# Optimization experiments

Hardware: AMD Instinct MI355X
Metric: run time of the kernel (lower is better)

## Reference

```python
import jax, jax.numpy as jnp
import numpy as np

N_NODES = 50000
N_EDGES = 800000
D_IN = 96
D_HID = 256
D_OUT = 2
N_GRAPHS = 64


def _gin_conv(x, src, dst, W1, b1, W2, b2):
    # GINConv with eps=0: MLP(x + sum_{j in N(i)} x_j)
    agg = jax.ops.segment_sum(x[src], dst, num_segments=x.shape[0])
    h = x + agg
    h = jax.nn.relu(h @ W1 + b1)
    return h @ W2 + b2


def setup_inputs() -> dict:
    key = jax.random.key(0)
    ks = jax.random.split(key, 12)
    x = jax.random.normal(ks[0], (N_NODES, D_IN), dtype=jnp.float32)
    edge_index = jax.random.randint(ks[1], (2, N_EDGES), 0, N_NODES, dtype=jnp.int64)
    batch = jnp.sort(jax.random.randint(ks[2], (N_NODES,), 0, N_GRAPHS, dtype=jnp.int64))

    def lin(k, fan_in, shape):
        bound = 1.0 / np.sqrt(fan_in)
        return jax.random.uniform(k, shape, jnp.float32, -bound, bound)

    W1 = lin(ks[3], D_IN, (D_IN, D_HID)); b1 = lin(ks[4], D_IN, (D_HID,))
    W2 = lin(ks[5], D_HID, (D_HID, D_HID)); b2 = lin(ks[6], D_HID, (D_HID,))
    V1 = lin(ks[7], D_HID, (D_HID, D_HID)); c1 = lin(ks[8], D_HID, (D_HID,))
    V2 = lin(ks[9], D_HID, (D_HID, D_HID)); c2 = lin(ks[10], D_HID, (D_HID,))
    Wl = lin(ks[11], D_HID, (D_HID, D_OUT)); bl = jnp.zeros((D_OUT,), jnp.float32)
    return {"x": x, "edge_index": edge_index, "batch": batch,
            "W1": W1, "b1": b1, "W2": W2, "b2": b2,
            "V1": V1, "c1": c1, "V2": V2, "c2": c2,
            "Wl": Wl, "bl": bl}


def reference(x, edge_index, batch, W1, b1, W2, b2, V1, c1, V2, c2, Wl, bl):
    src, dst = edge_index[0], edge_index[1]
    h = jax.nn.relu(_gin_conv(x, src, dst, W1, b1, W2, b2))
    h = _gin_conv(h, src, dst, V1, c1, V2, c2)
    # global_mean_pool over batch ids
    sums = jax.ops.segment_sum(h, batch, num_segments=N_GRAPHS)
    counts = jax.ops.segment_sum(jnp.ones((h.shape[0], 1), h.dtype), batch,
                                 num_segments=N_GRAPHS)
    pooled = sums / jnp.maximum(counts, 1.0)
    # dropout p=0.1 is identity in eval mode
    return pooled @ Wl + bl
```

## Files before the change

### kernel.cpp

```cpp
#include <hip/hip_runtime.h>

#define N_NODES 50000
#define N_EDGES 800000
#define D_IN 96
#define D_HID 256
#define N_GRAPHS 64

#define SCAN_NB ((N_NODES + 255) / 256)

typedef __attribute__((ext_vector_type(8))) short bf16x8;
typedef __attribute__((ext_vector_type(4))) float f32x4;

__device__ __forceinline__ unsigned short f2bf(float f) {
    union { float f; unsigned int u; } v; v.f = f;
    unsigned int r = (v.u + 0x7FFFu + ((v.u >> 16) & 1u)) >> 16;
    return (unsigned short)r;
}
__device__ __forceinline__ float bfLo(unsigned int u) {
    union { unsigned int u; float f; } v; v.u = u << 16; return v.f;
}
__device__ __forceinline__ float bfHi(unsigned int u) {
    union { unsigned int u; float f; } v; v.u = u & 0xFFFF0000u; return v.f;
}
__device__ __forceinline__ unsigned int packbf(float a, float b) {
    return (unsigned int)f2bf(a) | ((unsigned int)f2bf(b) << 16);
}

__global__ void k_count(const int* __restrict__ dst, int* __restrict__ deg, int E) {
    int e = blockIdx.x * blockDim.x + threadIdx.x;
    if (e < E) atomicAdd(&deg[dst[e]], 1);
}

__global__ __launch_bounds__(256) void k_scan1(const int* __restrict__ deg,
                                               int* __restrict__ bsum, int n) {
    __shared__ int red[256];
    int tid = threadIdx.x;
    int i = blockIdx.x * 256 + tid;
    red[tid] = (i < n) ? deg[i] : 0;
    __syncthreads();
    for (int off = 128; off > 0; off >>= 1) {
        if (tid < off) red[tid] += red[tid + off];
        __syncthreads();
    }
    if (tid == 0) bsum[blockIdx.x] = red[0];
}

__global__ __launch_bounds__(256) void k_scan2(int* __restrict__ bsum, int nb) {
    __shared__ int s[256];
    int tid = threadIdx.x;
    int v = (tid < nb) ? bsum[tid] : 0;
    s[tid] = v;
    __syncthreads();
    for (int off = 1; off < 256; off <<= 1) {
        int t = (tid >= off) ? s[tid - off] : 0;
        __syncthreads();
        s[tid] += t;
        __syncthreads();
    }
    if (tid < nb) bsum[tid] = s[tid] - v;
}

__global__ __launch_bounds__(256) void k_scan3(const int* __restrict__ deg,
                                               const int* __restrict__ bsum,
                                               int* __restrict__ rp,
                                               int* __restrict__ wp, int n) {
    __shared__ int s[256];
    int tid = threadIdx.x;
    int i = blockIdx.x * 256 + tid;
    int v = (i < n) ? deg[i] : 0;
    s[tid] = v;
    __syncthreads();
    for (int off = 1; off < 256; off <<= 1) {
        int t = (tid >= off) ? s[tid - off] : 0;
        __syncthreads();
        s[tid] += t;
        __syncthreads();
    }
    if (i < n) {
        int excl = s[tid] - v + bsum[blockIdx.x];
        rp[i] = excl;
        wp[i] = excl;
    }
    if (blockIdx.x == 0 && tid == 0) rp[n] = N_EDGES;
}

__global__ __launch_bounds__(256) void k_scatter2(const int* __restrict__ src,
                                                  const int* __restrict__ dst,
                                                  int* __restrict__ wp,
                                                  int* __restrict__ csr, int E) {
    int range = blockIdx.x & 7;
    int chunk = blockIdx.x >> 3;
    int lo = range * (N_NODES / 8);
    int hi = (range == 7) ? N_NODES : lo + (N_NODES / 8);
    int per = (E + 255) / 256;
    int s = chunk * per;
    int e = s + per;
    if (e > E) e = E;
    for (int i = s + threadIdx.x; i < e; i += 256) {
        int d = dst[i];
        if (d >= lo && d < hi) {
            int p = atomicAdd(&wp[d], 1);
            csr[p] = src[i];
        }
    }
}

__global__ __launch_bounds__(256) void k_x2bf(const float* __restrict__ x,
                                              unsigned short* __restrict__ xb, int n4) {
    int i = blockIdx.x * 256 + threadIdx.x;
    if (i >= n4) return;
    float4 v = ((const float4*)x)[i];
    ((uint2*)xb)[i] = make_uint2(packbf(v.x, v.y), packbf(v.z, v.w));
}

#define ACCUM(acc, v)                                    \
    do {                                                 \
        acc[0] += bfLo((v).x); acc[1] += bfHi((v).x);    \
        acc[2] += bfLo((v).y); acc[3] += bfHi((v).y);    \
        acc[4] += bfLo((v).z); acc[5] += bfHi((v).z);    \
        acc[6] += bfLo((v).w); acc[7] += bfHi((v).w);    \
    } while (0)

__global__ __launch_bounds__(256) void k_agg96b(const unsigned short* __restrict__ xb,
                                                const int* __restrict__ rp,
                                                const int* __restrict__ csr,
                                                unsigned short* __restrict__ h0, int n) {
    int wid = blockIdx.x * 4 + (threadIdx.x >> 6);
    if (wid >= n) return;
    int lane = threadIdx.x & 63;
    int grp = lane / 12;
    int sub = lane % 12;
    int s = rp[wid], e = rp[wid + 1];
    const uint4* xp = (const uint4*)xb;
    float a[8] = {0.f, 0.f, 0.f, 0.f, 0.f, 0.f, 0.f, 0.f};
    float b[8] = {0.f, 0.f, 0.f, 0.f, 0.f, 0.f, 0.f, 0.f};
    if (lane < 48) {
        int j = s + grp;
        for (; j + 4 < e; j += 8) {
            int sc0 = csr[j];
            int sc1 = csr[j + 4];
            uint4 v0 = xp[(size_t)sc0 * 12 + sub];
            uint4 v1 = xp[(size_t)sc1 * 12 + sub];
            ACCUM(a, v0);
            ACCUM(b, v1);
        }
        if (j < e) {
            int sc0 = csr[j];
            uint4 v0 = xp[(size_t)sc0 * 12 + sub];
            ACCUM(a, v0);
        }
    }
#pragma unroll
    for (int i = 0; i < 8; i++) a[i] += b[i];
#pragma unroll
    for (int i = 0; i < 8; i++) a[i] += __shfl(a[i], lane + 24, 64);
#pragma unroll
    for (int i = 0; i < 8; i++) a[i] += __shfl(a[i], lane + 12, 64);
    if (lane < 12) {
        uint4 v = xp[(size_t)wid * 12 + sub];
        ACCUM(a, v);
        uint4 o;
        o.x = packbf(a[0], a[1]); o.y = packbf(a[2], a[3]);
        o.z = packbf(a[4], a[5]); o.w = packbf(a[6], a[7]);
        ((uint4*)h0)[(size_t)wid * 12 + sub] = o;
    }
}

__global__ __launch_bounds__(256) void k_agg256b(const unsigned short* __restrict__ h,
                                                 const int* __restrict__ rp,
                                                 const int* __restrict__ csr,
                                                 unsigned short* __restrict__ outb, int n) {
    int wid = blockIdx.x * 4 + (threadIdx.x >> 6);
    if (wid >= n) return;
    int lane = threadIdx.x & 63;
    int half = lane >> 5;
    int sub = lane & 31;
    int s = rp[wid], e = rp[wid + 1];
    const uint4* hp = (const uint4*)h;
    float a[8] = {0.f, 0.f, 0.f, 0.f, 0.f, 0.f, 0.f, 0.f};
    float b[8] = {0.f, 0.f, 0.f, 0.f, 0.f, 0.f, 0.f, 0.f};
    int j = s + half;
    for (; j + 2 < e; j += 4) {
        int sc0 = csr[j];
        int sc1 = csr[j + 2];
        uint4 v0 = hp[(size_t)sc0 * 32 + sub];
        uint4 v1 = hp[(size_t)sc1 * 32 + sub];
        ACCUM(a, v0);
        ACCUM(b, v1);
    }
    if (j < e) {
        int sc0 = csr[j];
        uint4 v0 = hp[(size_t)sc0 * 32 + sub];
        ACCUM(a, v0);
    }
#pragma unroll
    for (int i = 0; i < 8; i++) a[i] += b[i];
#pragma unroll
    for (int i = 0; i < 8; i++) a[i] += __shfl(a[i], sub + 32, 64);
    if (half == 0) {
        uint4 v = hp[(size_t)wid * 32 + sub];
        ACCUM(a, v);
        uint4 o;
        o.x = packbf(a[0], a[1]); o.y = packbf(a[2], a[3]);
        o.z = packbf(a[4], a[5]); o.w = packbf(a[6], a[7]);
        ((uint4*)outb)[(size_t)wid * 32 + sub] = o;
    }
}

__global__ __launch_bounds__(256) void k_wt_all(const float* __restrict__ W1,
                                                const float* __restrict__ W2,
                                                const float* __restrict__ V1,
                                                const float* __restrict__ V2,
                                                unsigned short* __restrict__ wt1,
                                                unsigned short* __restrict__ wt2,
                                                unsigned short* __restrict__ wv1,
                                                unsigned short* __restrict__ wv2) {
    int idx = blockIdx.x * 256 + threadIdx.x;
    if (idx < D_IN * 256) {
        int k = idx >> 8, n = idx & 255;
        wt1[(size_t)n * D_IN + k] = f2bf(W1[idx]);
        return;
    }
    idx -= D_IN * 256;
    int mat = idx >> 16;
    int r = idx & 65535;
    int k = r >> 8, n = r & 255;
    const float* Ws = (mat == 0) ? W2 : (mat == 1) ? V1 : V2;
    unsigned short* Ds = (mat == 0) ? wt2 : (mat == 1) ? wv1 : wv2;
    Ds[(size_t)n * 256 + k] = f2bf(Ws[r]);
}

template <int K, bool RELU, bool OUTBF>
__global__ __launch_bounds__(256) void gemm_mfma(const unsigned short* __restrict__ A,
                                                 const unsigned short* __restrict__ Wt,
                                                 const float* __restrict__ bias,
                                                 void* __restrict__ Cv, int M) {
    constexpr int BM = 64, BN = 128, BK = 64;
    __shared__ unsigned short As[BM][BK + 8];
    __shared__ unsigned short Bs[BN][BK + 8];
    const int tid = threadIdx.x;
    const int lane = tid & 63;
    const int wid = tid >> 6;
    const int wm = wid >> 1;
    const int wn = wid & 1;

    const int nrb = (M + 63) >> 6;
    const int nfull2 = ((nrb >> 3) << 3) * 2;
    int bid = blockIdx.x;
    int rblk, halfc;
    if (bid < nfull2) {
        int g = bid >> 4, w = bid & 15;
        halfc = w >> 3;
        rblk = g * 8 + (w & 7);
    } else {
        int idx = bid - nfull2;
        int rem = nrb - (nfull2 >> 1);
        rblk = (nfull2 >> 1) + (idx % rem);
        halfc = idx / rem;
    }
    const int row0 = rblk * BM;
    const int col0 = halfc * BN;

    f32x4 acc[2][4];
#pragma unroll
    for (int f = 0; f < 2; f++)
#pragma unroll
        for (int g = 0; g < 4; g++) acc[f][g] = (f32x4){0.f, 0.f, 0.f, 0.f};

    for (int kt = 0; kt < K; kt += BK) {
        __syncthreads();
        {
            int m = tid >> 2;
            int kc = (tid & 3) * 16;
            int gr = row0 + m;
            uint4 w0 = make_uint4(0u, 0u, 0u, 0u), w1 = w0;
            int k = kt + kc;
            if (gr < M && k < K) {
                w0 = *(const uint4*)&A[(size_t)gr * K + k];
                if (k + 8 < K) w1 = *(const uint4*)&A[(size_t)gr * K + k + 8];
            }
            uint4* dst = (uint4*)&As[m][kc];
            dst[0] = w0; dst[1] = w1;
        }
        {
            int n = tid >> 1;
            int kc = (tid & 1) * 32;
            uint4 w[4];
#pragma unroll
            for (int i = 0; i < 4; i++) {
                int k = kt + kc + i * 8;
                if (k < K)
                    w[i] = *(const uint4*)&Wt[(size_t)(col0 + n) * K + k];
                else
                    w[i] = make_uint4(0u, 0u, 0u, 0u);
            }
            uint4* dst = (uint4*)&Bs[n][kc];
#pragma unroll
            for (int i = 0; i < 4; i++) dst[i] = w[i];
        }
        __syncthreads();
#pragma unroll
        for (int ks = 0; ks < 2; ks++) {
            int ko = ks * 32 + (lane >> 4) * 8;
            bf16x8 af[2], bfr[4];
#pragma unroll
            for (int f = 0; f < 2; f++)
                af[f] = *(const bf16x8*)&As[wm * 32 + f * 16 + (lane & 15)][ko];
#pragma unroll
            for (int g = 0; g < 4; g++)
                bfr[g] = *(const bf16x8*)&Bs[wn * 64 + g * 16 + (lane & 15)][ko];
#pragma unroll
            for (int f = 0; f < 2; f++)
#pragma unroll
                for (int g = 0; g < 4; g++)
                    acc[f][g] = __builtin_amdgcn_mfma_f32_16x16x32_bf16(
                        af[f], bfr[g], acc[f][g], 0, 0, 0);
        }
    }

#pragma unroll
    for (int g = 0; g < 4; g++) {
        int n = col0 + wn * 64 + g * 16 + (lane & 15);
        float bb = bias[n];
#pragma unroll
        for (int f = 0; f < 2; f++) {
#pragma unroll
            for (int r = 0; r < 4; r++) {
                int m = row0 + wm * 32 + f * 16 + (lane >> 4) * 4 + r;
                if (m < M) {
                    float v = acc[f][g][r] + bb;
                    if (RELU) v = fmaxf(v, 0.f);
                    if (OUTBF)
                        ((unsigned short*)Cv)[(size_t)m * 256 + n] = f2bf(v);
                    else
                        ((float*)Cv)[(size_t)m * 256 + n] = v;
                }
            }
        }
    }
}

#define POOL_ROWS 64
__global__ __launch_bounds__(256) void k_pool_partial(const unsigned short* __restrict__ h,
                                                      const int* __restrict__ batch,
                                                      float* __restrict__ psum, int n) {
    int r0 = blockIdx.x * POOL_ROWS;
    int r1 = r0 + POOL_ROWS;
    if (r1 > n) r1 = n;
    if (r0 >= r1) return;
    int c = threadIdx.x;
    float acc = 0.f;
    int g = batch[r0];
    for (int r = r0; r < r1; r++) {
        int gr = batch[r];
        if (gr != g) {
            atomicAdd(&psum[g * 256 + c], acc);
            acc = 0.f;
            g = gr;
        }
        acc += bfLo((unsigned int)h[(size_t)r * 256 + c]);
    }
    atomicAdd(&psum[g * 256 + c], acc);
}

__device__ __forceinline__ int lower_bound_i(const int* __restrict__ a, int n, int v) {
    int lo = 0, hi = n;
    while (lo < hi) {
        int mid = (lo + hi) >> 1;
        if (a[mid] < v) lo = mid + 1; else hi = mid;
    }
    return lo;
}

__global__ __launch_bounds__(128) void k_head(const float* __restrict__ psum,
                                              const int* __restrict__ batch,
                                              const float* __restrict__ Wl,
                                              const float* __restrict__ bl,
                                              float* __restrict__ out, int n) {
    int tid = threadIdx.x;
    int g = tid >> 1, o = tid & 1;
    int s = lower_bound_i(batch, n, g);
    int e = lower_bound_i(batch, n, g + 1);
    float inv = 1.0f / (float)((e - s) > 1 ? (e - s) : 1);
    float sum = bl[o];
    for (int k = 0; k < 256; k++)
        sum = fmaf(psum[g * 256 + k] * inv, Wl[k * 2 + o], sum);
    out[g * 2 + o] = sum;
}

extern "C" void kernel_launch(void* const* d_in, const int* in_sizes, int n_in,
                              void* d_out, int out_size, void* d_ws, size_t ws_size,
                              hipStream_t stream) {
    const float* x = (const float*)d_in[0];
    const int* ei = (const int*)d_in[1];
    const int* batch = (const int*)d_in[2];
    const float* W1 = (const float*)d_in[3];
    const float* b1 = (const float*)d_in[4];
    const float* W2 = (const float*)d_in[5];
    const float* b2 = (const float*)d_in[6];
    const float* V1 = (const float*)d_in[7];
    const float* c1 = (const float*)d_in[8];
    const float* V2 = (const float*)d_in[9];
    const float* c2 = (const float*)d_in[10];
    const float* Wl = (const float*)d_in[11];
    const float* bl = (const float*)d_in[12];
    float* out = (float*)d_out;

    const int* srcp = ei;
    const int* dstp = ei + N_EDGES;

    char* ws = (char*)d_ws;
    size_t off = 0;
    auto alloc = [&](size_t bytes) {
        size_t o = off;
        off = (off + bytes + 255) & ~(size_t)255;
        return o;
    };
    size_t o_deg = alloc(sizeof(int) * (N_NODES + 1));
    size_t o_rp = alloc(sizeof(int) * (N_NODES + 1));
    size_t o_wp = alloc(sizeof(int) * (N_NODES + 1));
    size_t o_bsum = alloc(sizeof(int) * SCAN_NB);
    size_t o_csr = alloc(sizeof(int) * N_EDGES);
    size_t o_B1 = alloc(sizeof(unsigned short) * (size_t)N_NODES * D_HID);
    size_t o_B2 = alloc(sizeof(unsigned short) * (size_t)N_NODES * D_HID);
    size_t o_pool = alloc(sizeof(float) * N_GRAPHS * D_HID);
    size_t o_wt1 = alloc(sizeof(unsigned short) * D_IN * D_HID);
    size_t o_wt2 = alloc(sizeof(unsigned short) * D_HID * D_HID);
    size_t o_wv1 = alloc(sizeof(unsigned short) * D_HID * D_HID);
    size_t o_wv2 = alloc(sizeof(unsigned short) * D_HID * D_HID);
    (void)ws_size;

    int* deg = (int*)(ws + o_deg);
    int* rp = (int*)(ws + o_rp);
    int* wp = (int*)(ws + o_wp);
    int* bsum = (int*)(ws + o_bsum);
    int* csr = (int*)(ws + o_csr);
    unsigned short* B1 = (unsigned short*)(ws + o_B1);
    unsigned short* B2 = (unsigned short*)(ws + o_B2);
    float* psum = (float*)(ws + o_pool);
    unsigned short* wt1 = (unsigned short*)(ws + o_wt1);
    unsigned short* wt2 = (unsigned short*)(ws + o_wt2);
    unsigned short* wv1 = (unsigned short*)(ws + o_wv1);
    unsigned short* wv2 = (unsigned short*)(ws + o_wv2);

    hipMemsetAsync(deg, 0, sizeof(int) * (N_NODES + 1), stream);
    hipMemsetAsync(psum, 0, sizeof(float) * N_GRAPHS * D_HID, stream);

    k_wt_all<<<(D_IN * 256 + 3 * 65536 + 255) / 256, 256, 0, stream>>>(
        W1, W2, V1, V2, wt1, wt2, wv1, wv2);

    k_count<<<(N_EDGES + 255) / 256, 256, 0, stream>>>(dstp, deg, N_EDGES);
    k_scan1<<<SCAN_NB, 256, 0, stream>>>(deg, bsum, N_NODES);
    k_scan2<<<1, 256, 0, stream>>>(bsum, SCAN_NB);
    k_scan3<<<SCAN_NB, 256, 0, stream>>>(deg, bsum, rp, wp, N_NODES);
    k_scatter2<<<2048, 256, 0, stream>>>(srcp, dstp, wp, csr, N_EDGES);

    k_x2bf<<<(N_NODES * D_IN / 4 + 255) / 256, 256, 0, stream>>>(x, B1, N_NODES * D_IN / 4);

    int nrb = (N_NODES + 63) / 64;
    int ggrid = nrb * 2;

    k_agg96b<<<(N_NODES + 3) / 4, 256, 0, stream>>>(B1, rp, csr, B2, N_NODES);
    gemm_mfma<96, true, true><<<ggrid, 256, 0, stream>>>(B2, wt1, b1, B1, N_NODES);
    gemm_mfma<256, true, true><<<ggrid, 256, 0, stream>>>(B1, wt2, b2, B2, N_NODES);

    k_agg256b<<<(N_NODES + 3) / 4, 256, 0, stream>>>(B2, rp, csr, B1, N_NODES);
    gemm_mfma<256, true, true><<<ggrid, 256, 0, stream>>>(B1, wv1, c1, B2, N_NODES);
    gemm_mfma<256, false, true><<<ggrid, 256, 0, stream>>>(B2, wv2, c2, B1, N_NODES);

    k_pool_partial<<<(N_NODES + POOL_ROWS - 1) / POOL_ROWS, 256, 0, stream>>>(
        B1, batch, psum, N_NODES);
    k_head<<<1, 128, 0, stream>>>(psum, batch, Wl, bl, out, N_NODES);
}
```

Before: 315.4 us.

## Split 256-wide aggregation into 8 feature slices with 16 edge groups per wave

The 256-feature neighbor aggregation now launches 8 blocks per node group. Each wave handles one 64-byte feature slice (4 lanes of uint4) and spreads edges across 16 lane groups, then combines them with an xor-shuffle reduction. The aim is more memory-level parallelism per node, since 16 independent gathers are in flight instead of 2 per half-wave. The cost is 8x more waves, CSR indices re-read once per slice, and 64-byte gather segments instead of full 512-byte rows, which may lower coalescing efficiency.

```diff
diff --git a/kernel.cpp b/kernel.cpp
--- a/kernel.cpp
+++ b/kernel.cpp
@@ -166,44 +166,37 @@
     }
 }
 
-__global__ __launch_bounds__(256) void k_agg256b(const unsigned short* __restrict__ h,
+__global__ __launch_bounds__(256) void k_agg256s(const unsigned short* __restrict__ h,
                                                  const int* __restrict__ rp,
                                                  const int* __restrict__ csr,
                                                  unsigned short* __restrict__ outb, int n) {
-    int wid = blockIdx.x * 4 + (threadIdx.x >> 6);
+    int slice = blockIdx.x & 7;
+    int wid = (blockIdx.x >> 3) * 4 + (threadIdx.x >> 6);
     if (wid >= n) return;
     int lane = threadIdx.x & 63;
-    int half = lane >> 5;
-    int sub = lane & 31;
+    int eg = lane >> 2;
+    int sub = lane & 3;
     int s = rp[wid], e = rp[wid + 1];
     const uint4* hp = (const uint4*)h;
+    int base = slice * 4 + sub;
     float a[8] = {0.f, 0.f, 0.f, 0.f, 0.f, 0.f, 0.f, 0.f};
-    float b[8] = {0.f, 0.f, 0.f, 0.f, 0.f, 0.f, 0.f, 0.f};
-    int j = s + half;
-    for (; j + 2 < e; j += 4) {
-        int sc0 = csr[j];
-        int sc1 = csr[j + 2];
-        uint4 v0 = hp[(size_t)sc0 * 32 + sub];
-        uint4 v1 = hp[(size_t)sc1 * 32 + sub];
-        ACCUM(a, v0);
-        ACCUM(b, v1);
-    }
-    if (j < e) {
-        int sc0 = csr[j];
-        uint4 v0 = hp[(size_t)sc0 * 32 + sub];
-        ACCUM(a, v0);
-    }
-#pragma unroll
-    for (int i = 0; i < 8; i++) a[i] += b[i];
-#pragma unroll
-    for (int i = 0; i < 8; i++) a[i] += __shfl(a[i], sub + 32, 64);
-    if (half == 0) {
-        uint4 v = hp[(size_t)wid * 32 + sub];
+    for (int j = s + eg; j < e; j += 16) {
+        int sc = csr[j];
+        uint4 v = hp[(size_t)sc * 32 + base];
+        ACCUM(a, v);
+    }
+#pragma unroll
+    for (int m = 4; m <= 32; m <<= 1) {
+#pragma unroll
+        for (int i = 0; i < 8; i++) a[i] += __shfl_xor(a[i], m, 64);
+    }
+    if (eg == 0) {
+        uint4 v = hp[(size_t)wid * 32 + base];
         ACCUM(a, v);
         uint4 o;
         o.x = packbf(a[0], a[1]); o.y = packbf(a[2], a[3]);
         o.z = packbf(a[4], a[5]); o.w = packbf(a[6], a[7]);
-        ((uint4*)outb)[(size_t)wid * 32 + sub] = o;
+        ((uint4*)outb)[(size_t)wid * 32 + base] = o;
     }
 }
 
@@ -464,7 +457,7 @@
     gemm_mfma<96, true, true><<<ggrid, 256, 0, stream>>>(B2, wt1, b1, B1, N_NODES);
     gemm_mfma<256, true, true><<<ggrid, 256, 0, stream>>>(B1, wt2, b2, B2, N_NODES);
 
-    k_agg256b<<<(N_NODES + 3) / 4, 256, 0, stream>>>(B2, rp, csr, B1, N_NODES);
+    k_agg256s<<<((N_NODES + 3) / 4) * 8, 256, 0, stream>>>(B2, rp, csr, B1, N_NODES);
     gemm_mfma<256, true, true><<<ggrid, 256, 0, stream>>>(B1, wv1, c1, B2, N_NODES);
     gemm_mfma<256, false, true><<<ggrid, 256, 0, stream>>>(B2, wv2, c2, B1, N_NODES);
 
```

After: 400.8 us. 27.1% more time.
